# Kernel tuning notes

Measured on AMD Instinct MI355X. Metric: run time of the kernel, lower is better.

Reference implementation:

```python
import jax, jax.numpy as jnp
import numpy as np

B, NP, KP = 1024, 196, 4  # batch, patches per image (14x14), pixels per patch
THR_HI, THR_LO, W_LO = 0.8, 0.5, 0.5


def setup_inputs() -> dict:
    key = jax.random.key(0)
    k1, k2, k3, k4 = jax.random.split(key, 4)
    x = jax.random.normal(k1, (B, 1, 28, 28), dtype=jnp.float32)
    phi = jax.random.uniform(k2, (B, NP, KP), dtype=jnp.float32) * (2.0 * np.pi)
    W_lin = jax.random.normal(k3, (10, NP * KP), dtype=jnp.float32) * 0.05
    b_lin = jax.random.normal(k4, (10,), dtype=jnp.float32) * 0.05
    return {"x": x, "phi": phi, "W_lin": W_lin, "b_lin": b_lin}


def _extract_patches(x):
    # x: [B,1,28,28] -> non-overlapping 2x2 patches, flatten order (kh, kw)
    b = x.shape[0]
    p = x[:, 0].reshape(b, 14, 2, 14, 2)            # (b, hp, kh, wp, kw)
    p = jnp.transpose(p, (0, 1, 3, 2, 4))           # (b, hp, wp, kh, kw)
    return p.reshape(b, NP, KP)


def _forward(x, phi, W_lin, b_lin):
    theta = _extract_patches(x)                     # [B,196,4] RY angles
    # Analytic 4-qubit circuit: z_i = <Z_i before CNOTs> = cos(theta)cos(phi);
    # CNOT chain maps Z_k -> Z_0...Z_k, so expvals are the cumulative product.
    z = jnp.cos(theta) * jnp.cos(phi)               # [B,196,4]
    expvals = jnp.cumprod(z, axis=-1)               # [B,196,4]

    # Graph is built on detached states in the original (patch_out.detach())
    states = jax.lax.stop_gradient(expvals)
    nrm = states / (jnp.linalg.norm(states, axis=-1, keepdims=True) + 1e-12)
    fid = jnp.einsum("bnd,bmd->bnm", nrm, nrm) ** 2  # squared cosine fidelity
    w = jnp.where(fid >= THR_HI, 1.0, jnp.where(fid >= THR_LO, W_LO, 0.0))
    w = w * (1.0 - jnp.eye(NP, dtype=w.dtype))       # no self-edges (i<j pairs)
    deg = jnp.sum(w, axis=-1)                        # [B,196]
    # smooth = I + L, L = D - W
    smooth = jnp.eye(NP, dtype=w.dtype)[None] + (jnp.zeros_like(w) + jnp.eye(NP)[None] * deg[:, :, None] - w)
    smoothed = jnp.einsum("bnm,bmd->bnd", smooth, expvals)  # [B,196,4]

    feats = smoothed.reshape(smoothed.shape[0], -1)  # [B,784]
    logits = feats @ W_lin.T + b_lin
    return jax.nn.log_softmax(logits, axis=-1)


def reference(x, phi, W_lin, b_lin):
    return _forward(x, phi, W_lin, b_lin)
```

## Files before the change

kernel.cpp:

```cpp
#include <hip/hip_runtime.h>
#include <math.h>

#define NP 196
#define NCLS 10

__global__ __launch_bounds__(256, 4) void quanv_fused_kernel(
    const float* __restrict__ x,
    const float* __restrict__ phi,
    const float* __restrict__ W,
    const float* __restrict__ bl,
    float* __restrict__ out)
{
    const int b    = blockIdx.x;
    const int t    = threadIdx.x;
    const int wave = t >> 6;
    const int lane = t & 63;

    __shared__ float4 e_s[NP];
    __shared__ float  inv_s[NP];
    __shared__ float2 thr_s[NP];
    __shared__ float4 pa_s[4 * NP];
    __shared__ float  pd_s[4 * NP];
    __shared__ float4 feat_s[NP];
    __shared__ float  logit_s[NCLS];

    const float* xb = x + (size_t)b * 784;
    const float* pb = phi + (size_t)b * 784;

    if (t < NP) {
        const int hp = t / 14, wp = t - hp * 14;
        const int r0 = hp * 2, c0 = wp * 2;
        float th0 = xb[r0 * 28 + c0];
        float th1 = xb[r0 * 28 + c0 + 1];
        float th2 = xb[(r0 + 1) * 28 + c0];
        float th3 = xb[(r0 + 1) * 28 + c0 + 1];
        float4 ph = *(const float4*)(pb + t * 4);
        float z0 = __cosf(th0) * __cosf(ph.x);
        float z1 = __cosf(th1) * __cosf(ph.y);
        float z2 = __cosf(th2) * __cosf(ph.z);
        float z3 = __cosf(th3) * __cosf(ph.w);
        float e0 = z0;
        float e1 = e0 * z1;
        float e2 = e1 * z2;
        float e3 = e2 * z3;
        e_s[t] = make_float4(e0, e1, e2, e3);
        float nn = sqrtf(e0 * e0 + e1 * e1 + e2 * e2 + e3 * e3) + 1e-12f;
        inv_s[t] = 1.0f / nn;
        thr_s[t] = make_float2(0.8944271909999159f * nn,
                               0.7071067811865476f * nn);
    }
    __syncthreads();

    float4 qn[3];
    float4 a[3];
    float  deg[3];
    #pragma unroll
    for (int k = 0; k < 3; ++k) {
        const int n = lane + 64 * k;
        float4 q = e_s[n];
        float iv = inv_s[n];
        qn[k] = make_float4(q.x * iv, q.y * iv, q.z * iv, q.w * iv);
        a[k] = make_float4(0.f, 0.f, 0.f, 0.f);
        deg[k] = 0.f;
    }
    const int m0 = wave * 49;
    #pragma unroll 7
    for (int m = m0; m < m0 + 49; ++m) {
        float4 em = e_s[m];
        float2 th = thr_s[m];
        #pragma unroll
        for (int k = 0; k < 3; ++k) {
            float d  = qn[k].x * em.x + qn[k].y * em.y + qn[k].z * em.z + qn[k].w * em.w;
            float ad = fabsf(d);
            float w  = (ad >= th.x) ? 1.0f : ((ad >= th.y) ? 0.5f : 0.0f);
            deg[k] += w;
            a[k].x += w * em.x;
            a[k].y += w * em.y;
            a[k].z += w * em.z;
            a[k].w += w * em.w;
        }
    }
    #pragma unroll
    for (int k = 0; k < 3; ++k) {
        pa_s[wave * NP + lane + 64 * k] = a[k];
        pd_s[wave * NP + lane + 64 * k] = deg[k];
    }

    {
        const int nt    = 192 + (lane & 3);
        const int slice = lane >> 2;
        float4 q = e_s[nt];
        float iv = inv_s[nt];
        float4 qt = make_float4(q.x * iv, q.y * iv, q.z * iv, q.w * iv);
        float4 at = make_float4(0.f, 0.f, 0.f, 0.f);
        float  dt = 0.f;
        for (int m = m0 + slice; m < m0 + 49; m += 16) {
            float4 em = e_s[m];
            float2 th = thr_s[m];
            float d  = qt.x * em.x + qt.y * em.y + qt.z * em.z + qt.w * em.w;
            float ad = fabsf(d);
            float w  = (ad >= th.x) ? 1.0f : ((ad >= th.y) ? 0.5f : 0.0f);
            dt += w;
            at.x += w * em.x;
            at.y += w * em.y;
            at.z += w * em.z;
            at.w += w * em.w;
        }
        #pragma unroll
        for (int off = 4; off <= 32; off <<= 1) {
            at.x += __shfl_xor(at.x, off, 64);
            at.y += __shfl_xor(at.y, off, 64);
            at.z += __shfl_xor(at.z, off, 64);
            at.w += __shfl_xor(at.w, off, 64);
            dt   += __shfl_xor(dt,   off, 64);
        }
        if (lane < 4) {
            pa_s[wave * NP + 192 + lane] = at;
            pd_s[wave * NP + 192 + lane] = dt;
        }
    }
    __syncthreads();

    if (t < NP) {
        float4 e  = e_s[t];
        float  iv = inv_s[t];
        float2 th = thr_s[t];
        float4 at = make_float4(0.f, 0.f, 0.f, 0.f);
        float  dt = 0.f;
        #pragma unroll
        for (int w = 0; w < 4; ++w) {
            float4 p = pa_s[w * NP + t];
            at.x += p.x; at.y += p.y; at.z += p.z; at.w += p.w;
            dt += pd_s[w * NP + t];
        }
        float qx = e.x * iv, qy = e.y * iv, qz = e.z * iv, qw = e.w * iv;
        float d  = qx * e.x + qy * e.y + qz * e.z + qw * e.w;
        float ad = fabsf(d);
        float w  = (ad >= th.x) ? 1.0f : ((ad >= th.y) ? 0.5f : 0.0f);
        dt -= w;
        at.x -= w * e.x; at.y -= w * e.y; at.z -= w * e.z; at.w -= w * e.w;
        const float s = 1.0f + dt;
        feat_s[t] = make_float4(s * e.x - at.x, s * e.y - at.y,
                                s * e.z - at.z, s * e.w - at.w);
    }
    __syncthreads();

    if (t < NCLS * 16) {
        const int j  = t >> 4;
        const int sl = t & 15;
        const float4* wr = (const float4*)(W + j * 784);
        float p = 0.f;
        for (int i = sl; i < NP; i += 16) {
            float4 f  = feat_s[i];
            float4 w4 = wr[i];
            p += f.x * w4.x + f.y * w4.y + f.z * w4.z + f.w * w4.w;
        }
        #pragma unroll
        for (int off = 8; off > 0; off >>= 1)
            p += __shfl_down(p, off, 16);
        if (sl == 0) logit_s[j] = p + bl[j];
    }
    __syncthreads();

    if (t < NCLS) {
        float mx = -INFINITY;
        #pragma unroll
        for (int j = 0; j < NCLS; ++j) mx = fmaxf(mx, logit_s[j]);
        float sum = 0.f;
        #pragma unroll
        for (int j = 0; j < NCLS; ++j) sum += expf(logit_s[j] - mx);
        out[(size_t)b * NCLS + t] = logit_s[t] - mx - logf(sum);
    }
}

extern "C" void kernel_launch(void* const* d_in, const int* in_sizes, int n_in,
                              void* d_out, int out_size, void* d_ws, size_t ws_size,
                              hipStream_t stream) {
    const float* x   = (const float*)d_in[0];
    const float* phi = (const float*)d_in[1];
    const float* W   = (const float*)d_in[2];
    const float* bl  = (const float*)d_in[3];
    float* out = (float*)d_out;

    const int B = in_sizes[0] / 784;
    quanv_fused_kernel<<<dim3(B), dim3(256), 0, stream>>>(x, phi, W, bl, out);
}
```

Baseline: 22.48 us.

## Map one image per wavefront and remove block-level syncs and shared reductions

Each block now processes four images, one per 64-lane wavefront, instead of one image per 256-thread block. Each wave computes the full 196x196 pairwise graph for its own image. This drops the cross-wave partial-sum buffers and every __syncthreads. The linear layer and log-softmax are done with wave shuffles, with the features kept in registers. In exchange each wave does four times the serial inner-loop work, and the grid shrinks to B/4 blocks (256 for B=1024), which may leave CUs underused. The launch assumes B is divisible by 4.

```diff
diff --git a/kernel.cpp b/kernel.cpp
--- a/kernel.cpp
+++ b/kernel.cpp
@@ -4,99 +4,111 @@
 #define NP 196
 #define NCLS 10
 
-__global__ __launch_bounds__(256, 4) void quanv_fused_kernel(
+__global__ __launch_bounds__(256) void quanv_fused_kernel(
     const float* __restrict__ x,
     const float* __restrict__ phi,
     const float* __restrict__ W,
     const float* __restrict__ bl,
     float* __restrict__ out)
 {
-    const int b    = blockIdx.x;
     const int t    = threadIdx.x;
     const int wave = t >> 6;
     const int lane = t & 63;
+    const int img  = blockIdx.x * 4 + wave;
 
-    __shared__ float4 e_s[NP];
-    __shared__ float  inv_s[NP];
-    __shared__ float2 thr_s[NP];
-    __shared__ float4 pa_s[4 * NP];
-    __shared__ float  pd_s[4 * NP];
-    __shared__ float4 feat_s[NP];
-    __shared__ float  logit_s[NCLS];
+    __shared__ float4 e_s[4][NP];
+    __shared__ float  inv_s[4][NP];
+    __shared__ float2 thr_s[4][NP];
 
-    const float* xb = x + (size_t)b * 784;
-    const float* pb = phi + (size_t)b * 784;
+    const float* xb = x + (size_t)img * 784;
+    const float* pb = phi + (size_t)img * 784;
 
-    if (t < NP) {
-        const int hp = t / 14, wp = t - hp * 14;
-        const int r0 = hp * 2, c0 = wp * 2;
-        float th0 = xb[r0 * 28 + c0];
-        float th1 = xb[r0 * 28 + c0 + 1];
-        float th2 = xb[(r0 + 1) * 28 + c0];
-        float th3 = xb[(r0 + 1) * 28 + c0 + 1];
-        float4 ph = *(const float4*)(pb + t * 4);
-        float z0 = __cosf(th0) * __cosf(ph.x);
-        float z1 = __cosf(th1) * __cosf(ph.y);
-        float z2 = __cosf(th2) * __cosf(ph.z);
-        float z3 = __cosf(th3) * __cosf(ph.w);
-        float e0 = z0;
-        float e1 = e0 * z1;
-        float e2 = e1 * z2;
-        float e3 = e2 * z3;
-        e_s[t] = make_float4(e0, e1, e2, e3);
-        float nn = sqrtf(e0 * e0 + e1 * e1 + e2 * e2 + e3 * e3) + 1e-12f;
-        inv_s[t] = 1.0f / nn;
-        thr_s[t] = make_float2(0.8944271909999159f * nn,
-                               0.7071067811865476f * nn);
+    #pragma unroll
+    for (int pass = 0; pass < 4; ++pass) {
+        const int p = lane + 64 * pass;
+        if (pass < 3 || lane < 4) {
+            const int hp = p / 14, wp = p - hp * 14;
+            const int r0 = hp * 2, c0 = wp * 2;
+            float th0 = xb[r0 * 28 + c0];
+            float th1 = xb[r0 * 28 + c0 + 1];
+            float th2 = xb[(r0 + 1) * 28 + c0];
+            float th3 = xb[(r0 + 1) * 28 + c0 + 1];
+            float4 ph = *(const float4*)(pb + p * 4);
+            float z0 = __cosf(th0) * __cosf(ph.x);
+            float z1 = __cosf(th1) * __cosf(ph.y);
+            float z2 = __cosf(th2) * __cosf(ph.z);
+            float z3 = __cosf(th3) * __cosf(ph.w);
+            float e0 = z0;
+            float e1 = e0 * z1;
+            float e2 = e1 * z2;
+            float e3 = e2 * z3;
+            e_s[wave][p] = make_float4(e0, e1, e2, e3);
+            float nn = sqrtf(e0 * e0 + e1 * e1 + e2 * e2 + e3 * e3) + 1e-12f;
+            inv_s[wave][p] = 1.0f / nn;
+            thr_s[wave][p] = make_float2(0.8944271909999159f * nn,
+                                         0.7071067811865476f * nn);
+        }
     }
-    __syncthreads();
 
-    float4 qn[3];
-    float4 a[3];
-    float  deg[3];
-    #pragma unroll
-    for (int k = 0; k < 3; ++k) {
-        const int n = lane + 64 * k;
-        float4 q = e_s[n];
-        float iv = inv_s[n];
-        qn[k] = make_float4(q.x * iv, q.y * iv, q.z * iv, q.w * iv);
-        a[k] = make_float4(0.f, 0.f, 0.f, 0.f);
-        deg[k] = 0.f;
-    }
-    const int m0 = wave * 49;
-    #pragma unroll 7
-    for (int m = m0; m < m0 + 49; ++m) {
-        float4 em = e_s[m];
-        float2 th = thr_s[m];
+    float4 f[3];
+    {
+        float4 qn[3];
+        float4 a[3];
+        float  deg[3];
         #pragma unroll
         for (int k = 0; k < 3; ++k) {
-            float d  = qn[k].x * em.x + qn[k].y * em.y + qn[k].z * em.z + qn[k].w * em.w;
+            const int n = lane + 64 * k;
+            float4 q = e_s[wave][n];
+            float iv = inv_s[wave][n];
+            qn[k] = make_float4(q.x * iv, q.y * iv, q.z * iv, q.w * iv);
+            a[k] = make_float4(0.f, 0.f, 0.f, 0.f);
+            deg[k] = 0.f;
+        }
+        #pragma unroll 7
+        for (int m = 0; m < NP; ++m) {
+            float4 em = e_s[wave][m];
+            float2 th = thr_s[wave][m];
+            #pragma unroll
+            for (int k = 0; k < 3; ++k) {
+                float d  = qn[k].x * em.x + qn[k].y * em.y + qn[k].z * em.z + qn[k].w * em.w;
+                float ad = fabsf(d);
+                float w  = (ad >= th.x) ? 1.0f : ((ad >= th.y) ? 0.5f : 0.0f);
+                deg[k] += w;
+                a[k].x += w * em.x;
+                a[k].y += w * em.y;
+                a[k].z += w * em.z;
+                a[k].w += w * em.w;
+            }
+        }
+        #pragma unroll
+        for (int k = 0; k < 3; ++k) {
+            const int n = lane + 64 * k;
+            float4 e  = e_s[wave][n];
+            float  iv = inv_s[wave][n];
+            float2 th = thr_s[wave][n];
+            float d  = (e.x * iv) * e.x + (e.y * iv) * e.y + (e.z * iv) * e.z + (e.w * iv) * e.w;
             float ad = fabsf(d);
             float w  = (ad >= th.x) ? 1.0f : ((ad >= th.y) ? 0.5f : 0.0f);
-            deg[k] += w;
-            a[k].x += w * em.x;
-            a[k].y += w * em.y;
-            a[k].z += w * em.z;
-            a[k].w += w * em.w;
+            deg[k] -= w;
+            a[k].x -= w * e.x; a[k].y -= w * e.y; a[k].z -= w * e.z; a[k].w -= w * e.w;
+            const float s = 1.0f + deg[k];
+            f[k] = make_float4(s * e.x - a[k].x, s * e.y - a[k].y,
+                               s * e.z - a[k].z, s * e.w - a[k].w);
         }
     }
-    #pragma unroll
-    for (int k = 0; k < 3; ++k) {
-        pa_s[wave * NP + lane + 64 * k] = a[k];
-        pd_s[wave * NP + lane + 64 * k] = deg[k];
-    }
 
+    float4 ft;
+    const int nt = 192 + (lane & 3);
     {
-        const int nt    = 192 + (lane & 3);
         const int slice = lane >> 2;
-        float4 q = e_s[nt];
-        float iv = inv_s[nt];
+        float4 q = e_s[wave][nt];
+        float iv = inv_s[wave][nt];
         float4 qt = make_float4(q.x * iv, q.y * iv, q.z * iv, q.w * iv);
         float4 at = make_float4(0.f, 0.f, 0.f, 0.f);
         float  dt = 0.f;
-        for (int m = m0 + slice; m < m0 + 49; m += 16) {
-            float4 em = e_s[m];
-            float2 th = thr_s[m];
+        for (int m = slice; m < NP; m += 16) {
+            float4 em = e_s[wave][m];
+            float2 th = thr_s[wave][m];
             float d  = qt.x * em.x + qt.y * em.y + qt.z * em.z + qt.w * em.w;
             float ad = fabsf(d);
             float w  = (ad >= th.x) ? 1.0f : ((ad >= th.y) ? 0.5f : 0.0f);
@@ -114,62 +126,55 @@
             at.w += __shfl_xor(at.w, off, 64);
             dt   += __shfl_xor(dt,   off, 64);
         }
-        if (lane < 4) {
-            pa_s[wave * NP + 192 + lane] = at;
-            pd_s[wave * NP + 192 + lane] = dt;
-        }
-    }
-    __syncthreads();
-
-    if (t < NP) {
-        float4 e  = e_s[t];
-        float  iv = inv_s[t];
-        float2 th = thr_s[t];
-        float4 at = make_float4(0.f, 0.f, 0.f, 0.f);
-        float  dt = 0.f;
-        #pragma unroll
-        for (int w = 0; w < 4; ++w) {
-            float4 p = pa_s[w * NP + t];
-            at.x += p.x; at.y += p.y; at.z += p.z; at.w += p.w;
-            dt += pd_s[w * NP + t];
-        }
-        float qx = e.x * iv, qy = e.y * iv, qz = e.z * iv, qw = e.w * iv;
-        float d  = qx * e.x + qy * e.y + qz * e.z + qw * e.w;
+        float2 th = thr_s[wave][nt];
+        float d  = qt.x * q.x + qt.y * q.y + qt.z * q.z + qt.w * q.w;
         float ad = fabsf(d);
         float w  = (ad >= th.x) ? 1.0f : ((ad >= th.y) ? 0.5f : 0.0f);
         dt -= w;
-        at.x -= w * e.x; at.y -= w * e.y; at.z -= w * e.z; at.w -= w * e.w;
+        at.x -= w * q.x; at.y -= w * q.y; at.z -= w * q.z; at.w -= w * q.w;
         const float s = 1.0f + dt;
-        feat_s[t] = make_float4(s * e.x - at.x, s * e.y - at.y,
-                                s * e.z - at.z, s * e.w - at.w);
+        ft = make_float4(s * q.x - at.x, s * q.y - at.y,
+                         s * q.z - at.z, s * q.w - at.w);
     }
-    __syncthreads();
 
-    if (t < NCLS * 16) {
-        const int j  = t >> 4;
-        const int sl = t & 15;
+    float pj[NCLS];
+    #pragma unroll
+    for (int j = 0; j < NCLS; ++j) {
         const float4* wr = (const float4*)(W + j * 784);
         float p = 0.f;
-        for (int i = sl; i < NP; i += 16) {
-            float4 f  = feat_s[i];
-            float4 w4 = wr[i];
-            p += f.x * w4.x + f.y * w4.y + f.z * w4.z + f.w * w4.w;
+        #pragma unroll
+        for (int k = 0; k < 3; ++k) {
+            const int n = lane + 64 * k;
+            float4 w4 = wr[n];
+            p += f[k].x * w4.x + f[k].y * w4.y + f[k].z * w4.z + f[k].w * w4.w;
         }
+        if (lane < 4) {
+            float4 w4 = wr[nt];
+            p += ft.x * w4.x + ft.y * w4.y + ft.z * w4.z + ft.w * w4.w;
+        }
+        pj[j] = p;
+    }
+    #pragma unroll
+    for (int j = 0; j < NCLS; ++j) {
+        float v = pj[j];
         #pragma unroll
-        for (int off = 8; off > 0; off >>= 1)
-            p += __shfl_down(p, off, 16);
-        if (sl == 0) logit_s[j] = p + bl[j];
+        for (int off = 32; off > 0; off >>= 1)
+            v += __shfl_xor(v, off, 64);
+        pj[j] = v;
     }
-    __syncthreads();
 
-    if (t < NCLS) {
+    if (lane < NCLS) {
+        float lg[NCLS];
         float mx = -INFINITY;
         #pragma unroll
-        for (int j = 0; j < NCLS; ++j) mx = fmaxf(mx, logit_s[j]);
+        for (int j = 0; j < NCLS; ++j) {
+            lg[j] = pj[j] + bl[j];
+            mx = fmaxf(mx, lg[j]);
+        }
         float sum = 0.f;
         #pragma unroll
-        for (int j = 0; j < NCLS; ++j) sum += expf(logit_s[j] - mx);
-        out[(size_t)b * NCLS + t] = logit_s[t] - mx - logf(sum);
+        for (int j = 0; j < NCLS; ++j) sum += expf(lg[j] - mx);
+        out[(size_t)img * NCLS + lane] = lg[lane] - mx - logf(sum);
     }
 }
 
@@ -183,5 +188,5 @@
     float* out = (float*)d_out;
 
     const int B = in_sizes[0] / 784;
-    quanv_fused_kernel<<<dim3(B), dim3(256), 0, stream>>>(x, phi, W, bl, out);
+    quanv_fused_kernel<<<dim3(B / 4), dim3(256), 0, stream>>>(x, phi, W, bl, out);
 }
```

Result: slower. 24.41 us (+8.6%).
